# Optimization experiments

Measured on AMD Instinct MI355X. Metric: run time of the kernel, lower is better.

## Reference

```python
import jax, jax.numpy as jnp
import numpy as np

N = 50000
E = 1600000
D_CONTENT, D_STYLE, D_CAT = 768, 128, 32  # concat feature = 2*D_CAT = 64
H1, H2, NCLS = 64, 64, 2


def _lin_params(key, din, dout, bias=True):
    k1, k2 = jax.random.split(key)
    s = 1.0 / np.sqrt(din)
    W = jax.random.uniform(k1, (din, dout), jnp.float32, -s, s)
    b = jax.random.uniform(k2, (dout,), jnp.float32, -s, s) if bias else None
    return W, b


def setup_inputs() -> dict:
    key = jax.random.key(0)
    ks = jax.random.split(key, 16)
    x_content = jax.random.normal(ks[0], (N, D_CONTENT), jnp.float32)
    x_style = jax.random.normal(ks[1], (N, D_STYLE), jnp.float32)
    edge_index = jax.random.randint(ks[2], (2, E), 0, N, jnp.int64)
    edge_type = jax.random.randint(ks[3], (E,), 0, 4, jnp.int64)
    Wp, bp = _lin_params(ks[4], D_CONTENT, D_CAT)
    Ws, bs = _lin_params(ks[5], D_STYLE, D_CAT)
    # SAGEConv: lin_l (aggregated neighbors, has bias), lin_r (root, no bias)
    Wl1, bl1 = _lin_params(ks[6], 2 * D_CAT, H1)
    Wr1, _ = _lin_params(ks[7], 2 * D_CAT, H1, bias=False)
    Wl2, bl2 = _lin_params(ks[8], H1, H2)
    Wr2, _ = _lin_params(ks[9], H1, H2, bias=False)
    Wl3, bl3 = _lin_params(ks[10], H2, H2)
    Wr3, _ = _lin_params(ks[11], H2, H2, bias=False)
    Wo, bo = _lin_params(ks[12], H2, NCLS)
    return dict(x_content=x_content, x_style=x_style, edge_index=edge_index,
                edge_type=edge_type, Wp=Wp, bp=bp, Ws=Ws, bs=bs,
                Wl1=Wl1, bl1=bl1, Wr1=Wr1, Wl2=Wl2, bl2=bl2, Wr2=Wr2,
                Wl3=Wl3, bl3=bl3, Wr3=Wr3, Wo=Wo, bo=bo)


def _sage_conv(x, src, dst, Wl, bl, Wr):
    # mean aggregation of source-node features at destination nodes
    msg_sum = jax.ops.segment_sum(x[src], dst, num_segments=N)  # [N, d]
    deg = jax.ops.segment_sum(jnp.ones((src.shape[0],), x.dtype), dst,
                              num_segments=N)
    agg = msg_sum / jnp.maximum(deg, 1.0)[:, None]
    return agg @ Wl + bl + x @ Wr


def reference(x_content, x_style, edge_index, edge_type,
              Wp, bp, Ws, bs, Wl1, bl1, Wr1, Wl2, bl2, Wr2,
              Wl3, bl3, Wr3, Wo, bo):
    src, dst = edge_index[0], edge_index[1]
    x = jnp.concatenate([x_content @ Wp + bp, x_style @ Ws + bs], axis=1)
    x = jax.nn.relu(_sage_conv(x, src, dst, Wl1, bl1, Wr1))  # dropout = id (eval)
    x = jax.nn.relu(_sage_conv(x, src, dst, Wl2, bl2, Wr2))
    x = jax.nn.relu(_sage_conv(x, src, dst, Wl3, bl3, Wr3))
    return x @ Wo + bo
```

## Files before the change

kernel.cpp:

```cpp
#include <hip/hip_runtime.h>
#include <stdint.h>


typedef __attribute__((ext_vector_type(8))) unsigned short u16x8;
typedef __attribute__((ext_vector_type(8))) short bf16x8;
typedef __attribute__((ext_vector_type(4))) float f32x4;
typedef __attribute__((ext_vector_type(4))) unsigned int u32x4;
typedef __attribute__((ext_vector_type(2))) int i32x2;

static __device__ __forceinline__ float bf2f(unsigned short u) {
  union { unsigned int i; float f; } v;
  v.i = ((unsigned int)u) << 16;
  return v.f;
}

static __device__ __forceinline__ unsigned short f2bf(float f) {
  union { float f; unsigned int i; } v;
  v.f = f;
  unsigned int u = v.i;
  unsigned int r = (u + 0x7FFFu + ((u >> 16) & 1u)) >> 16;
  return (unsigned short)r;
}

template <bool BF>
static __device__ __forceinline__ float ldf(const void* p, long long i) {
  if (BF) return bf2f(((const unsigned short*)p)[i]);
  return ((const float*)p)[i];
}

static __device__ __forceinline__ int clampN(int v, int N) {
  return v < 0 ? 0 : (v >= N ? N - 1 : v);
}

__global__ void k_detect(const void* Wp, const int* ei, int* flags) {
  if (threadIdx.x == 0 && blockIdx.x == 0) {
    const unsigned short* w = (const unsigned short*)Wp;
    int bf = 1;
    for (int i = 0; i < 64; ++i) {
      float v = fabsf(bf2f(w[i]));
      if (!(v < 1.0f)) bf = 0;
    }
    flags[0] = bf;
    int i64 = 1;
    for (int i = 0; i < 32; ++i)
      if (ei[2 * i + 1] != 0) i64 = 0;
    flags[1] = i64;
  }
}

static __device__ __forceinline__ int edge_src(const int* ei, int e, int E,
                                               int i64) {
  return i64 ? ei[2 * (long long)e] : ei[e];
}
static __device__ __forceinline__ int edge_dst(const int* ei, int e, int E,
                                               int i64) {
  return i64 ? ei[2 * ((long long)E + e)] : ei[(long long)E + e];
}


__global__ __launch_bounds__(256) void k_pack(const int* __restrict__ ei, int E,
                                              int N, int* __restrict__ cnt,
                                              i32x2* __restrict__ pairs,
                                              const int* __restrict__ flags) {
  int e = blockIdx.x * 256 + threadIdx.x;
  if (e < E) {
    int i64 = flags[1];
    int s = clampN(edge_src(ei, e, E, i64), N);
    int d = clampN(edge_dst(ei, e, E, i64), N);
    i32x2 p;
    p[0] = s;
    p[1] = d;
    pairs[e] = p;
    atomicAdd(&cnt[d], 1);
  }
}

__global__ __launch_bounds__(256) void k_scan1(const int* __restrict__ cnt,
                                               int* __restrict__ rowptr,
                                               int* __restrict__ bsum, int N) {
  __shared__ int sh[256];
  int t = threadIdx.x;
  int base = blockIdx.x * 1024 + t * 4;
  int v0 = 0, v1 = 0, v2 = 0, v3 = 0;
  if (base + 0 < N) v0 = cnt[base + 0];
  if (base + 1 < N) v1 = cnt[base + 1];
  if (base + 2 < N) v2 = cnt[base + 2];
  if (base + 3 < N) v3 = cnt[base + 3];
  int s = v0 + v1 + v2 + v3;
  sh[t] = s;
  __syncthreads();
  int acc = s;
  for (int off = 1; off < 256; off <<= 1) {
    int x = 0;
    if (t >= off) x = sh[t - off];
    __syncthreads();
    acc += x;
    sh[t] = acc;
    __syncthreads();
  }
  int run = acc - s;
  if (base + 0 < N) rowptr[base + 0] = run;
  run += v0;
  if (base + 1 < N) rowptr[base + 1] = run;
  run += v1;
  if (base + 2 < N) rowptr[base + 2] = run;
  run += v2;
  if (base + 3 < N) rowptr[base + 3] = run;
  run += v3;
  if (t == 255) bsum[blockIdx.x] = acc;
}

__global__ void k_scan2(int* __restrict__ bsum, int nb,
                        int* __restrict__ rowptr, int N) {
  if (threadIdx.x == 0 && blockIdx.x == 0) {
    int run = 0;
    for (int i = 0; i < nb; ++i) {
      int v = bsum[i];
      bsum[i] = run;
      run += v;
    }
    rowptr[N] = run;
  }
}

__global__ __launch_bounds__(256) void k_scan3(int* __restrict__ rowptr,
                                               int* __restrict__ cursor,
                                               const int* __restrict__ bsum,
                                               int N) {
  int i = blockIdx.x * 256 + threadIdx.x;
  if (i < N) {
    int v = rowptr[i] + bsum[i >> 10];
    rowptr[i] = v;
    cursor[i] = v;
  }
}

__global__ __launch_bounds__(256) void k_scatter2(
    const i32x2* __restrict__ pairs, int E, int lo, int hi,
    int* __restrict__ cursor, int* __restrict__ colbuf) {
  int e = blockIdx.x * 256 + threadIdx.x;
  if (e < E) {
    i32x2 p2 = pairs[e];
    int d = p2[1];
    if (d >= lo && d < hi) {
      int p = atomicAdd(&cursor[d], 1);
      if (p >= 0 && p < E) colbuf[p] = p2[0];
    }
  }
}

static __device__ void project_mfma(const void* __restrict__ xc,
                                    const void* __restrict__ xs,
                                    const void* __restrict__ Wp,
                                    const void* __restrict__ bp,
                                    const void* __restrict__ Ws,
                                    const void* __restrict__ bs,
                                    float* __restrict__ h0, int N,
                                    float* __restrict__ lds) {
  unsigned short* fb = (unsigned short*)lds;
  int tid = (int)threadIdx.x;
  int w = __builtin_amdgcn_readfirstlane(tid >> 6);
  int l = tid & 63;
  int node0 = (int)blockIdx.x * 64;

  const unsigned short* wp16 = (const unsigned short*)Wp;
  const unsigned short* ws16 = (const unsigned short*)Ws;
#pragma unroll
  for (int i = 0; i < 14; ++i) {
    int ci = tid + 256 * i;
    int e0 = ci * 8;
    int isC = e0 < 24576;
    int eb = isC ? e0 : (e0 - 24576);
    int r = eb >> 5;
    int c0 = eb & 31;
    int s_ = r >> 5;
    int g = (r >> 3) & 3;
    int j = r & 7;
    int f = isC ? (s_ * 2 + (c0 >> 4)) : (48 + s_ * 2 + (c0 >> 4));
    u16x8 v = *(const u16x8*)((isC ? wp16 : ws16) + eb);
    unsigned short* d = fb + f * 512 + ((g << 4) + (c0 & 15)) * 8 + j;
#pragma unroll
    for (int m = 0; m < 8; ++m) d[m * 8] = v[m];
  }
  __syncthreads();

  int arow = node0 + 16 * w + (l & 15);
  int arowc = arow < N ? arow : (N - 1);
  int kg = (l >> 4) * 8;
  const unsigned short* xcl = (const unsigned short*)xc + (long long)arowc * 768;
  const unsigned short* xsl = (const unsigned short*)xs + (long long)arowc * 128;

  auto loadA = [&](int s) -> bf16x8 {
    if (s < 24) return *(const bf16x8*)(xcl + s * 32 + kg);
    return *(const bf16x8*)(xsl + (s - 24) * 32 + kg);
  };

  f32x4 ac0 = {0.f, 0.f, 0.f, 0.f};
  f32x4 ac1 = {0.f, 0.f, 0.f, 0.f};
  f32x4 ac2 = {0.f, 0.f, 0.f, 0.f};
  f32x4 ac3 = {0.f, 0.f, 0.f, 0.f};

  bf16x8 a0 = loadA(0);
  bf16x8 a1 = loadA(1);
#pragma unroll 1
  for (int s = 0; s < 28; ++s) {
    bf16x8 acur = a0;
    a0 = a1;
    if (s + 2 < 28) a1 = loadA(s + 2);
    if (s < 24) {
      bf16x8 b0 = *(const bf16x8*)(fb + (s * 2 + 0) * 512 + l * 8);
      bf16x8 b1 = *(const bf16x8*)(fb + (s * 2 + 1) * 512 + l * 8);
      ac0 = __builtin_amdgcn_mfma_f32_16x16x32_bf16(acur, b0, ac0, 0, 0, 0);
      ac1 = __builtin_amdgcn_mfma_f32_16x16x32_bf16(acur, b1, ac1, 0, 0, 0);
    } else {
      int sb = s - 24;
      bf16x8 b2 = *(const bf16x8*)(fb + (48 + sb * 2 + 0) * 512 + l * 8);
      bf16x8 b3 = *(const bf16x8*)(fb + (48 + sb * 2 + 1) * 512 + l * 8);
      ac2 = __builtin_amdgcn_mfma_f32_16x16x32_bf16(acur, b2, ac2, 0, 0, 0);
      ac3 = __builtin_amdgcn_mfma_f32_16x16x32_bf16(acur, b3, ac3, 0, 0, 0);
    }
  }

  int colb = l & 15;
  int rbase = (l >> 4) * 4;
#pragma unroll
  for (int r = 0; r < 4; ++r) {
    int nodeg = node0 + 16 * w + rbase + r;
    if (nodeg < N) {
      float* orow = h0 + (long long)nodeg * 64;
      orow[0 + colb] = ac0[r] + bf2f(((const unsigned short*)bp)[0 + colb]);
      orow[16 + colb] = ac1[r] + bf2f(((const unsigned short*)bp)[16 + colb]);
      orow[32 + colb] = ac2[r] + bf2f(((const unsigned short*)bs)[0 + colb]);
      orow[48 + colb] = ac3[r] + bf2f(((const unsigned short*)bs)[16 + colb]);
    }
  }
}

static __device__ void project_f32(const void* __restrict__ xc,
                                   const void* __restrict__ xs,
                                   const void* __restrict__ Wp,
                                   const void* __restrict__ bp,
                                   const void* __restrict__ Ws,
                                   const void* __restrict__ bs,
                                   float* __restrict__ h0, int N,
                                   float* __restrict__ lds) {
  float* xt = lds;
  float* wtf = lds + 2 * 64 * 68;

  int tid = (int)threadIdx.x;
  int w = __builtin_amdgcn_readfirstlane(tid >> 6);
  int lane = tid & 63;
  int node = (int)blockIdx.x * 64 + lane;

  int sn = tid >> 2;
  int sj = tid & 3;
  int gsn = (int)blockIdx.x * 64 + sn;
  int gsnc = gsn < N ? gsn : (N - 1);

  float c[8], s[8];
#pragma unroll
  for (int r = 0; r < 8; ++r) {
    c[r] = 0.f;
    s[r] = 0.f;
  }

  f32x4 pf0 = {}, pf1 = {}, pf2 = {}, pf3 = {};
  f32x4 wf0 = {}, wf1 = {};

  auto stage_load = [&](int t) {
    long long idx;
    const void* src;
    if (t < 12) {
      src = xc;
      idx = (long long)gsnc * 768 + t * 64 + 16 * sj;
    } else {
      src = xs;
      idx = (long long)gsnc * 128 + (t - 12) * 64 + 16 * sj;
    }
    const float* p = (const float*)src + idx;
    pf0 = *(const f32x4*)(p + 0);
    pf1 = *(const f32x4*)(p + 4);
    pf2 = *(const f32x4*)(p + 8);
    pf3 = *(const f32x4*)(p + 12);
    int rowg = (t < 12) ? (t * 64 + sn) : ((t - 12) * 64 + sn);
    const float* wp = (const float*)((t < 12) ? Wp : Ws) +
                      (long long)rowg * 32 + 8 * sj;
    wf0 = *(const f32x4*)wp;
    wf1 = *(const f32x4*)(wp + 4);
  };

  auto stage_write = [&](int t) {
    float* row = xt + (t & 1) * (64 * 68) + sn * 68 + 16 * sj;
    *(f32x4*)(row + 0) = pf0;
    *(f32x4*)(row + 4) = pf1;
    *(f32x4*)(row + 8) = pf2;
    *(f32x4*)(row + 12) = pf3;
    float* wrow = wtf + (t & 1) * (64 * 32) + sn * 32 + 8 * sj;
    *(f32x4*)wrow = wf0;
    *(f32x4*)(wrow + 4) = wf1;
  };

  stage_load(0);
  stage_write(0);
  __syncthreads();

#pragma unroll 1
  for (int t = 0; t < 14; ++t) {
    if (t + 1 < 14) stage_load(t + 1);
    const float* xrow = xt + (t & 1) * (64 * 68) + lane * 68;
    const float* wbase = wtf + (t & 1) * (64 * 32) + 8 * w;
    float* acc = (t < 12) ? c : s;
#pragma unroll 2
    for (int k0 = 0; k0 < 64; k0 += 4) {
      f32x4 x4 = *(const f32x4*)(xrow + k0);
#pragma unroll
      for (int kk = 0; kk < 4; ++kk) {
        const float* wr = wbase + (k0 + kk) * 32;
        f32x4 wa = *(const f32x4*)wr;
        f32x4 wb = *(const f32x4*)(wr + 4);
#pragma unroll
        for (int r = 0; r < 4; ++r) {
          acc[r] += x4[kk] * wa[r];
          acc[4 + r] += x4[kk] * wb[r];
        }
      }
    }
    if (t + 1 < 14) stage_write(t + 1);
    __syncthreads();
  }

  if (node < N) {
    float* orow = h0 + (long long)node * 64;
    f32x4 v;
#pragma unroll
    for (int r = 0; r < 4; ++r) v[r] = c[r] + ((const float*)bp)[8 * w + r];
    *(f32x4*)(orow + 8 * w) = v;
#pragma unroll
    for (int r = 0; r < 4; ++r)
      v[r] = c[4 + r] + ((const float*)bp)[8 * w + 4 + r];
    *(f32x4*)(orow + 8 * w + 4) = v;
#pragma unroll
    for (int r = 0; r < 4; ++r) v[r] = s[r] + ((const float*)bs)[8 * w + r];
    *(f32x4*)(orow + 32 + 8 * w) = v;
#pragma unroll
    for (int r = 0; r < 4; ++r)
      v[r] = s[4 + r] + ((const float*)bs)[8 * w + 4 + r];
    *(f32x4*)(orow + 32 + 8 * w + 4) = v;
  }
}

__global__ __launch_bounds__(256) void k_project(
    const void* __restrict__ xc, const void* __restrict__ xs,
    const void* __restrict__ Wp, const void* __restrict__ bp,
    const void* __restrict__ Ws, const void* __restrict__ bs,
    float* __restrict__ h0, int N, const int* __restrict__ flags) {
  __shared__ float lds[14336];
  if (flags[0])
    project_mfma(xc, xs, Wp, bp, Ws, bs, h0, N, lds);
  else
    project_f32(xc, xs, Wp, bp, Ws, bs, h0, N, lds);
}

template <bool BF>
static __device__ void layer_body(const float* __restrict__ hin,
                                  const int* __restrict__ rowptr,
                                  const int* __restrict__ colbuf,
                                  const void* Wl, const void* bl,
                                  const void* Wr, float* __restrict__ hout,
                                  int N, int last, const void* Wo,
                                  const void* bo, void* outp) {
  int node = (int)((blockIdx.x * blockDim.x + threadIdx.x) >> 6);
  int lane = (int)(threadIdx.x & 63);
  if (node >= N) return;
  int rs = rowptr[node], re = rowptr[node + 1];
  float xself = hin[(long long)node * 64 + lane];
  float agg0 = 0.f, agg1 = 0.f, agg2 = 0.f, agg3 = 0.f;
  float agg4 = 0.f, agg5 = 0.f, agg6 = 0.f, agg7 = 0.f;
  for (int cb = rs; cb < re; cb += 64) {
    int sidx = 0;
    if (cb + lane < re) sidx = clampN(colbuf[cb + lane], N);
    int c = re - cb;
    if (c > 64) c = 64;
    int t = 0;
    for (; t + 16 <= c; t += 16) {
      int s0 = __builtin_amdgcn_readlane(sidx, t + 0);
      int s1 = __builtin_amdgcn_readlane(sidx, t + 1);
      int s2 = __builtin_amdgcn_readlane(sidx, t + 2);
      int s3 = __builtin_amdgcn_readlane(sidx, t + 3);
      int s4 = __builtin_amdgcn_readlane(sidx, t + 4);
      int s5 = __builtin_amdgcn_readlane(sidx, t + 5);
      int s6 = __builtin_amdgcn_readlane(sidx, t + 6);
      int s7 = __builtin_amdgcn_readlane(sidx, t + 7);
      int s8 = __builtin_amdgcn_readlane(sidx, t + 8);
      int s9 = __builtin_amdgcn_readlane(sidx, t + 9);
      int sa = __builtin_amdgcn_readlane(sidx, t + 10);
      int sb = __builtin_amdgcn_readlane(sidx, t + 11);
      int sc = __builtin_amdgcn_readlane(sidx, t + 12);
      int sd = __builtin_amdgcn_readlane(sidx, t + 13);
      int se = __builtin_amdgcn_readlane(sidx, t + 14);
      int sf = __builtin_amdgcn_readlane(sidx, t + 15);
      float v0 = hin[(long long)s0 * 64 + lane];
      float v1 = hin[(long long)s1 * 64 + lane];
      float v2 = hin[(long long)s2 * 64 + lane];
      float v3 = hin[(long long)s3 * 64 + lane];
      float v4 = hin[(long long)s4 * 64 + lane];
      float v5 = hin[(long long)s5 * 64 + lane];
      float v6 = hin[(long long)s6 * 64 + lane];
      float v7 = hin[(long long)s7 * 64 + lane];
      float v8 = hin[(long long)s8 * 64 + lane];
      float v9 = hin[(long long)s9 * 64 + lane];
      float va = hin[(long long)sa * 64 + lane];
      float vb = hin[(long long)sb * 64 + lane];
      float vc = hin[(long long)sc * 64 + lane];
      float vd = hin[(long long)sd * 64 + lane];
      float ve = hin[(long long)se * 64 + lane];
      float vf = hin[(long long)sf * 64 + lane];
      agg0 += v0 + v8;
      agg1 += v1 + v9;
      agg2 += v2 + va;
      agg3 += v3 + vb;
      agg4 += v4 + vc;
      agg5 += v5 + vd;
      agg6 += v6 + ve;
      agg7 += v7 + vf;
    }
    for (; t + 8 <= c; t += 8) {
      int s0 = __builtin_amdgcn_readlane(sidx, t + 0);
      int s1 = __builtin_amdgcn_readlane(sidx, t + 1);
      int s2 = __builtin_amdgcn_readlane(sidx, t + 2);
      int s3 = __builtin_amdgcn_readlane(sidx, t + 3);
      int s4 = __builtin_amdgcn_readlane(sidx, t + 4);
      int s5 = __builtin_amdgcn_readlane(sidx, t + 5);
      int s6 = __builtin_amdgcn_readlane(sidx, t + 6);
      int s7 = __builtin_amdgcn_readlane(sidx, t + 7);
      float v0 = hin[(long long)s0 * 64 + lane];
      float v1 = hin[(long long)s1 * 64 + lane];
      float v2 = hin[(long long)s2 * 64 + lane];
      float v3 = hin[(long long)s3 * 64 + lane];
      float v4 = hin[(long long)s4 * 64 + lane];
      float v5 = hin[(long long)s5 * 64 + lane];
      float v6 = hin[(long long)s6 * 64 + lane];
      float v7 = hin[(long long)s7 * 64 + lane];
      agg0 += v0;
      agg1 += v1;
      agg2 += v2;
      agg3 += v3;
      agg4 += v4;
      agg5 += v5;
      agg6 += v6;
      agg7 += v7;
    }
    for (; t < c; ++t) {
      int s = __builtin_amdgcn_readlane(sidx, t);
      agg0 += hin[(long long)s * 64 + lane];
    }
  }
  float agg = ((agg0 + agg1) + (agg2 + agg3)) + ((agg4 + agg5) + (agg6 + agg7));
  int deg = re - rs;
  if (deg > 0) agg *= (1.f / (float)deg);

  float o = ldf<BF>(bl, lane);
#pragma unroll 8
  for (int d = 0; d < 64; ++d) {
    float ad = __uint_as_float(
        __builtin_amdgcn_readlane(__float_as_uint(agg), d));
    float xd = __uint_as_float(
        __builtin_amdgcn_readlane(__float_as_uint(xself), d));
    o += ad * ldf<BF>(Wl, d * 64 + lane);
    o += xd * ldf<BF>(Wr, d * 64 + lane);
  }
  o = fmaxf(o, 0.f);

  if (!last) {
    hout[(long long)node * 64 + lane] = o;
  } else {
    float c0 = o * ldf<BF>(Wo, lane * 2 + 0);
    float c1 = o * ldf<BF>(Wo, lane * 2 + 1);
    for (int off = 32; off > 0; off >>= 1) {
      c0 += __shfl_xor(c0, off, 64);
      c1 += __shfl_xor(c1, off, 64);
    }
    if (lane == 0) {
      float r0 = c0 + ldf<BF>(bo, 0);
      float r1 = c1 + ldf<BF>(bo, 1);
      if (BF) {
        unsigned short* o16 = (unsigned short*)outp;
        o16[(long long)node * 2 + 0] = f2bf(r0);
        o16[(long long)node * 2 + 1] = f2bf(r1);
      } else {
        float* o32 = (float*)outp;
        o32[(long long)node * 2 + 0] = r0;
        o32[(long long)node * 2 + 1] = r1;
      }
    }
  }
}

__global__ __launch_bounds__(256) void k_layer(
    const float* hin, const int* rowptr, const int* colbuf, const void* Wl,
    const void* bl, const void* Wr, float* hout, int N, int last,
    const void* Wo, const void* bo, void* outp, const int* __restrict__ flags) {
  if (flags[0])
    layer_body<true>(hin, rowptr, colbuf, Wl, bl, Wr, hout, N, last, Wo, bo,
                     outp);
  else
    layer_body<false>(hin, rowptr, colbuf, Wl, bl, Wr, hout, N, last, Wo, bo,
                      outp);
}


extern "C" void kernel_launch(void* const* d_in, const int* in_sizes, int n_in,
                              void* d_out, int out_size, void* d_ws,
                              size_t ws_size, hipStream_t stream) {
  const void* xc = d_in[0];
  const void* xs = d_in[1];
  const int* ei = (const int*)d_in[2];
  const void* Wp = d_in[4];
  const void* bp = d_in[5];
  const void* Ws = d_in[6];
  const void* bs = d_in[7];
  const void* Wl1 = d_in[8];
  const void* bl1 = d_in[9];
  const void* Wr1 = d_in[10];
  const void* Wl2 = d_in[11];
  const void* bl2 = d_in[12];
  const void* Wr2 = d_in[13];
  const void* Wl3 = d_in[14];
  const void* bl3 = d_in[15];
  const void* Wr3 = d_in[16];
  const void* Wo = d_in[17];
  const void* bo = d_in[18];

  int N = out_size / 2;
  int E = in_sizes[3];

  char* ws = (char*)d_ws;
  size_t off = 0;
  auto alloc = [&](size_t bytes) {
    char* p = ws + off;
    off += (bytes + 255) & ~(size_t)255;
    return p;
  };
  int* colbuf = (int*)alloc((size_t)E * 4);
  int* cnt = (int*)alloc((size_t)N * 4);
  int* rowptr = (int*)alloc((size_t)(N + 1) * 4);
  int* cursor = (int*)alloc((size_t)N * 4);
  int* bsum = (int*)alloc(4096);
  int* flags = (int*)alloc(256);
  float* h0 = (float*)alloc((size_t)N * 64 * 4);
  float* h1 = (float*)alloc((size_t)N * 64 * 4);
  (void)ws_size;
  (void)n_in;

  i32x2* pairs = (i32x2*)h0;

  k_detect<<<1, 64, 0, stream>>>(Wp, ei, flags);

  hipMemsetAsync(cnt, 0, (size_t)N * 4, stream);
  int eb = (E + 255) / 256;
  k_pack<<<eb, 256, 0, stream>>>(ei, E, N, cnt, pairs, flags);
  int sb = (N + 1023) / 1024;
  k_scan1<<<sb, 256, 0, stream>>>(cnt, rowptr, bsum, N);
  k_scan2<<<1, 64, 0, stream>>>(bsum, sb, rowptr, N);
  k_scan3<<<(N + 255) / 256, 256, 0, stream>>>(rowptr, cursor, bsum, N);

  const int NPASS = 4;
  int chunk = (N + NPASS - 1) / NPASS;
  for (int r = 0; r < NPASS; ++r) {
    int lo = r * chunk;
    int hi = lo + chunk < N ? lo + chunk : N;
    k_scatter2<<<eb, 256, 0, stream>>>(pairs, E, lo, hi, cursor, colbuf);
  }

  int pb = (N + 63) / 64;
  k_project<<<pb, 256, 0, stream>>>(xc, xs, Wp, bp, Ws, bs, h0, N, flags);

  int nb4 = (N + 3) / 4;
  k_layer<<<nb4, 256, 0, stream>>>(h0, rowptr, colbuf, Wl1, bl1, Wr1, h1, N, 0,
                                   nullptr, nullptr, nullptr, flags);
  k_layer<<<nb4, 256, 0, stream>>>(h1, rowptr, colbuf, Wl2, bl2, Wr2, h0, N, 0,
                                   nullptr, nullptr, nullptr, flags);
  k_layer<<<nb4, 256, 0, stream>>>(h0, rowptr, colbuf, Wl3, bl3, Wr3, h1, N, 1,
                                   Wo, bo, d_out, flags);
}
```

Baseline: 727.6 us.

## Prebuild MFMA weight fragments once and split projection into bf16/f32 kernels

Moves the per-block weight swizzle into a separate k_wprep kernel that writes fragment-ordered weights to workspace once. The projection blocks then do a plain vectorized copy into LDS. Blocks grow to 512 threads covering 128 nodes, and the A-operand prefetch depth rises from 2 to 4 with a fully unrolled loop. The mfma and f32 paths become separate kernels that early-exit on the flag, which costs one extra empty-grid launch and an extra launch for weight prep.

```diff
diff --git a/kernel.cpp b/kernel.cpp
--- a/kernel.cpp
+++ b/kernel.cpp
@@ -149,38 +149,46 @@
   }
 }
 
-static __device__ void project_mfma(const void* __restrict__ xc,
-                                    const void* __restrict__ xs,
-                                    const void* __restrict__ Wp,
-                                    const void* __restrict__ bp,
-                                    const void* __restrict__ Ws,
-                                    const void* __restrict__ bs,
-                                    float* __restrict__ h0, int N,
-                                    float* __restrict__ lds) {
-  unsigned short* fb = (unsigned short*)lds;
+__global__ __launch_bounds__(256) void k_wprep(const void* __restrict__ Wp,
+                                               const void* __restrict__ Ws,
+                                               unsigned short* __restrict__ wf,
+                                               const int* __restrict__ flags) {
+  if (!flags[0]) return;
+  int ci = (int)blockIdx.x * 256 + (int)threadIdx.x;
+  if (ci >= 3584) return;
+  int e0 = ci * 8;
+  int isC = e0 < 24576;
+  int eb = isC ? e0 : (e0 - 24576);
+  int r = eb >> 5;
+  int c0 = eb & 31;
+  int s_ = r >> 5;
+  int g = (r >> 3) & 3;
+  int j = r & 7;
+  int f = isC ? (s_ * 2 + (c0 >> 4)) : (48 + s_ * 2 + (c0 >> 4));
+  u16x8 v = *(const u16x8*)((const unsigned short*)(isC ? Wp : Ws) + eb);
+  unsigned short* d = wf + f * 512 + ((g << 4) + (c0 & 15)) * 8 + j;
+#pragma unroll
+  for (int m = 0; m < 8; ++m) d[m * 8] = v[m];
+}
+
+__global__ __launch_bounds__(512) void k_project_bf(
+    const void* __restrict__ xc, const void* __restrict__ xs,
+    const unsigned short* __restrict__ wf, const void* __restrict__ bp,
+    const void* __restrict__ bs, float* __restrict__ h0, int N,
+    const int* __restrict__ flags) {
+  __shared__ unsigned short fb[28672];
+  if (!flags[0]) return;
+
   int tid = (int)threadIdx.x;
   int w = __builtin_amdgcn_readfirstlane(tid >> 6);
   int l = tid & 63;
-  int node0 = (int)blockIdx.x * 64;
-
-  const unsigned short* wp16 = (const unsigned short*)Wp;
-  const unsigned short* ws16 = (const unsigned short*)Ws;
-#pragma unroll
-  for (int i = 0; i < 14; ++i) {
-    int ci = tid + 256 * i;
-    int e0 = ci * 8;
-    int isC = e0 < 24576;
-    int eb = isC ? e0 : (e0 - 24576);
-    int r = eb >> 5;
-    int c0 = eb & 31;
-    int s_ = r >> 5;
-    int g = (r >> 3) & 3;
-    int j = r & 7;
-    int f = isC ? (s_ * 2 + (c0 >> 4)) : (48 + s_ * 2 + (c0 >> 4));
-    u16x8 v = *(const u16x8*)((isC ? wp16 : ws16) + eb);
-    unsigned short* d = fb + f * 512 + ((g << 4) + (c0 & 15)) * 8 + j;
-#pragma unroll
-    for (int m = 0; m < 8; ++m) d[m * 8] = v[m];
+  int node0 = (int)blockIdx.x * 128;
+
+  {
+    const u32x4* src = (const u32x4*)wf;
+    u32x4* dst = (u32x4*)fb;
+#pragma unroll
+    for (int i = 0; i < 7; ++i) dst[tid + 512 * i] = src[tid + 512 * i];
   }
   __syncthreads();
 
@@ -200,13 +208,14 @@
   f32x4 ac2 = {0.f, 0.f, 0.f, 0.f};
   f32x4 ac3 = {0.f, 0.f, 0.f, 0.f};
 
-  bf16x8 a0 = loadA(0);
-  bf16x8 a1 = loadA(1);
-#pragma unroll 1
+  bf16x8 ap[4];
+#pragma unroll
+  for (int i = 0; i < 4; ++i) ap[i] = loadA(i);
+
+#pragma unroll
   for (int s = 0; s < 28; ++s) {
-    bf16x8 acur = a0;
-    a0 = a1;
-    if (s + 2 < 28) a1 = loadA(s + 2);
+    bf16x8 acur = ap[s & 3];
+    if (s + 4 < 28) ap[s & 3] = loadA(s + 4);
     if (s < 24) {
       bf16x8 b0 = *(const bf16x8*)(fb + (s * 2 + 0) * 512 + l * 8);
       bf16x8 b1 = *(const bf16x8*)(fb + (s * 2 + 1) * 512 + l * 8);
@@ -236,14 +245,14 @@
   }
 }
 
-static __device__ void project_f32(const void* __restrict__ xc,
-                                   const void* __restrict__ xs,
-                                   const void* __restrict__ Wp,
-                                   const void* __restrict__ bp,
-                                   const void* __restrict__ Ws,
-                                   const void* __restrict__ bs,
-                                   float* __restrict__ h0, int N,
-                                   float* __restrict__ lds) {
+__global__ __launch_bounds__(256) void k_project_f32(
+    const void* __restrict__ xc, const void* __restrict__ xs,
+    const void* __restrict__ Wp, const void* __restrict__ bp,
+    const void* __restrict__ Ws, const void* __restrict__ bs,
+    float* __restrict__ h0, int N, const int* __restrict__ flags) {
+  __shared__ float lds[2 * 64 * 68 + 2 * 64 * 32];
+  if (flags[0]) return;
+
   float* xt = lds;
   float* wtf = lds + 2 * 64 * 68;
 
@@ -347,18 +356,6 @@
       v[r] = s[4 + r] + ((const float*)bs)[8 * w + 4 + r];
     *(f32x4*)(orow + 32 + 8 * w + 4) = v;
   }
-}
-
-__global__ __launch_bounds__(256) void k_project(
-    const void* __restrict__ xc, const void* __restrict__ xs,
-    const void* __restrict__ Wp, const void* __restrict__ bp,
-    const void* __restrict__ Ws, const void* __restrict__ bs,
-    float* __restrict__ h0, int N, const int* __restrict__ flags) {
-  __shared__ float lds[14336];
-  if (flags[0])
-    project_mfma(xc, xs, Wp, bp, Ws, bs, h0, N, lds);
-  else
-    project_f32(xc, xs, Wp, bp, Ws, bs, h0, N, lds);
 }
 
 template <bool BF>
@@ -547,6 +544,7 @@
   int* cursor = (int*)alloc((size_t)N * 4);
   int* bsum = (int*)alloc(4096);
   int* flags = (int*)alloc(256);
+  unsigned short* wfrag = (unsigned short*)alloc(57344);
   float* h0 = (float*)alloc((size_t)N * 64 * 4);
   float* h1 = (float*)alloc((size_t)N * 64 * 4);
   (void)ws_size;
@@ -555,6 +553,8 @@
   i32x2* pairs = (i32x2*)h0;
 
   k_detect<<<1, 64, 0, stream>>>(Wp, ei, flags);
+
+  k_wprep<<<14, 256, 0, stream>>>(Wp, Ws, wfrag, flags);
 
   hipMemsetAsync(cnt, 0, (size_t)N * 4, stream);
   int eb = (E + 255) / 256;
@@ -572,8 +572,10 @@
     k_scatter2<<<eb, 256, 0, stream>>>(pairs, E, lo, hi, cursor, colbuf);
   }
 
-  int pb = (N + 63) / 64;
-  k_project<<<pb, 256, 0, stream>>>(xc, xs, Wp, bp, Ws, bs, h0, N, flags);
+  int pbB = (N + 127) / 128;
+  k_project_bf<<<pbB, 512, 0, stream>>>(xc, xs, wfrag, bp, bs, h0, N, flags);
+  int pbF = (N + 63) / 64;
+  k_project_f32<<<pbF, 256, 0, stream>>>(xc, xs, Wp, bp, Ws, bs, h0, N, flags);
 
   int nb4 = (N + 3) / 4;
   k_layer<<<nb4, 256, 0, stream>>>(h0, rowptr, colbuf, Wl1, bl1, Wr1, h1, N, 0,
```

Result: no change. 734.3 us (+0.9%).
